# Optimization experiments

Hardware: AMD Instinct MI355X
Metric: run time of the kernel (lower is better)

## Reference

```python
import jax, jax.numpy as jnp
import numpy as np

CM = 0.05   # collision_margin
NT = 4      # n_timesteps

def _lin(x, W, b):
    return x @ W + b

def _mlp2(x, W1, b1, W2, b2):
    return _lin(jax.nn.relu(_lin(x, W1, b1)), W2, b2)

def _mlp3(x, W1, b1, W2, b2, W3, b3):
    h = jax.nn.relu(_lin(x, W1, b1))
    h = jax.nn.relu(_lin(h, W2, b2))
    return _lin(h, W3, b3)

def _xavier(key, fan_in, fan_out):
    std = np.sqrt(2.0 / (fan_in + fan_out))
    return jax.random.normal(key, (fan_in, fan_out), dtype=jnp.float32) * std

def setup_inputs() -> dict:
    key = jax.random.key(0)
    ks = jax.random.split(key, 16)
    sd, h, es, ud, rd, gd = 8, 128, 128, 32, 64, 32
    B, N, T = 16, 64, 8
    inp = {
        'states': jax.random.normal(ks[0], (B, N, T, sd), dtype=jnp.float32),
        'temp': 1,
        # StateEncoder: Linear(sd,h)-ReLU-Linear(h,es)-ReLU
        'sW1': _xavier(ks[1], sd, h), 'sb1': jnp.zeros((h,), jnp.float32),
        'sW2': _xavier(ks[2], h, es), 'sb2': jnp.zeros((es,), jnp.float32),
        # InputEncoder (collision_margin path): Linear(sd,h)-ReLU-Linear(h,ud)
        'uW1': _xavier(ks[3], sd, h), 'ub1': jnp.zeros((h,), jnp.float32),
        'uW2': _xavier(ks[4], h, ud), 'ub2': jnp.zeros((ud,), jnp.float32),
        # InputPropagator: Linear(es+ud, ud)
        'upW': _xavier(ks[5], es + ud, ud), 'upb': jnp.zeros((ud,), jnp.float32),
        # RelationEncoder (collision_margin path): Linear(sd,h)-ReLU-Linear(h,rd)
        'reW1': _xavier(ks[6], sd, h), 'reb1': jnp.zeros((h,), jnp.float32),
        'reW2': _xavier(ks[7], h, rd), 'reb2': jnp.zeros((rd,), jnp.float32),
        # RelationPropagator: Linear(2*es+rd, rd)
        'rpW': _xavier(ks[8], 2 * es + rd, rd), 'rpb': jnp.zeros((rd,), jnp.float32),
        # ComposedEmbedding: Linear(es+ud+rd,h)-ReLU-Linear(h,h)-ReLU-Linear(h,gd)
        'cW1': _xavier(ks[9], es + ud + rd, h), 'cb1': jnp.zeros((h,), jnp.float32),
        'cW2': _xavier(ks[10], h, h), 'cb2': jnp.zeros((h,), jnp.float32),
        'cW3': _xavier(ks[11], h, gd), 'cb3': jnp.zeros((gd,), jnp.float32),
    }
    return inp

def reference(states, temp, sW1, sb1, sW2, sb2, uW1, ub1, uW2, ub2, upW, upb,
              reW1, reb1, reW2, reb2, rpW, rpb, cW1, cb1, cW2, cb2, cW3, cb3):
    B, N, T, sd = states.shape
    BT = B * T
    s = states.transpose(0, 2, 1, 3).reshape(BT, N, sd)  # [BT,N,sd]

    # node encoders
    enc_obj = jax.nn.relu(_mlp2(s, sW1, sb1, sW2, sb2))   # [BT,N,es]
    enc_u = _mlp2(s, uW1, ub1, uW2, ub2)                  # [BT,N,ud] (no relu in collision_margin path)
    # u mask (get_u_states_mask)
    u = ((jnp.abs(s[..., 0:1]) > 1 - CM) | (jnp.abs(s[..., NT:NT + 1]) > 1 - CM)).astype(s.dtype)

    obs_u = jax.nn.relu(_lin(jnp.concatenate([enc_obj, enc_u], axis=-1), upW, upb))  # [BT,N,ud]
    enc_comp = jnp.concatenate([enc_obj, obs_u], axis=-1)  # [BT,N,es+ud]

    # pairwise relations: receiver i (dim1), sender j (dim2)
    rel_states = s[:, :, None, :] - s[:, None, :, :]        # [BT,N,N,sd]
    enc_rel = jax.nn.relu(_mlp2(rel_states, reW1, reb1, reW2, reb2))  # [BT,N,N,rd]
    sel = ((jnp.abs(rel_states[..., 0:1]) > 2 * CM) |
           (jnp.abs(rel_states[..., NT:NT + 1]) > 2 * CM)).astype(s.dtype)  # [BT,N,N,1]

    es = enc_obj.shape[-1]
    recv = jnp.broadcast_to(enc_obj[:, :, None, :], (BT, N, N, es))
    send = jnp.broadcast_to(enc_obj[:, None, :, :], (BT, N, N, es))
    rel_in = jnp.concatenate([recv, send, enc_rel], axis=-1)            # [BT,N,N,2es+rd]
    rel_eff = jax.nn.relu(_lin(rel_in, rpW, rpb)) * sel                 # [BT,N,N,rd]
    rel_agg = rel_eff.sum(axis=2)                                       # scatter-sum over senders -> [BT,N,rd]

    enc_comp = jnp.concatenate([enc_comp, rel_agg], axis=-1)            # [BT,N,es+ud+rd]
    g = _mlp3(enc_comp, cW1, cb1, cW2, cb2, cW3, cb3)                   # [BT,N,gd]
    return g.reshape(B, T, N, -1)
```

## Files before the change

### kernel.cpp

```cpp
#include <hip/hip_runtime.h>
#include <hip/hip_bf16.h>


typedef __bf16 bf16x8 __attribute__((ext_vector_type(8)));
typedef float f32x4 __attribute__((ext_vector_type(4)));

__global__ __launch_bounds__(256) void k_prep(
    const float* __restrict__ sW1, const float* __restrict__ uW1,
    const float* __restrict__ reW1, const float* __restrict__ sW2,
    const float* __restrict__ uW2, const float* __restrict__ upW,
    const float* __restrict__ reW2, const float* __restrict__ rpW,
    const float* __restrict__ cW1, const float* __restrict__ cW2,
    const float* __restrict__ cW3,
    __bf16* __restrict__ Wl1f, __bf16* __restrict__ Ws2f,
    __bf16* __restrict__ Wu2f, __bf16* __restrict__ Wupf,
    __bf16* __restrict__ Wabf, __bf16* __restrict__ W2f,
    __bf16* __restrict__ Wbf,  __bf16* __restrict__ Wc1f,
    __bf16* __restrict__ Wc2f, __bf16* __restrict__ Wc3f)
{
    const int tid  = blockIdx.x * 256 + threadIdx.x;
    const int nthr = gridDim.x * 256;

#define PACK(dst, NKT, NCT, EXPR)                                   \
    for (int q = tid; q < (NKT) * (NCT) * 512; q += nthr) {         \
        const int f = q >> 9, rem = q & 511;                        \
        const int lane = rem >> 3, e = rem & 7;                     \
        const int kt = f / (NCT), ct = f % (NCT);                   \
        const int k = kt * 32 + (lane >> 4) * 8 + e;                \
        const int c = ct * 16 + (lane & 15);                        \
        (dst)[q] = (__bf16)(EXPR);                                  \
        (void)k; (void)c;                                           \
    }

    PACK(Wl1f, 1, 24, (k >= 8 ? 0.f :
        (c < 128 ? sW1[k * 128 + c] :
         c < 256 ? uW1[k * 128 + (c - 128)] : reW1[k * 128 + (c - 256)])))
    PACK(Ws2f, 4, 8, sW2[k * 128 + c])
    PACK(Wu2f, 4, 2, uW2[k * 32 + c])
    PACK(Wupf, 5, 2, (k < 160 ? upW[k * 32 + c] : 0.f))
    PACK(Wabf, 4, 8, (c < 64 ? rpW[k * 64 + c] : rpW[(128 + k) * 64 + (c - 64)]))
    PACK(W2f,  4, 4, reW2[k * 64 + c])
    PACK(Wbf,  2, 4, rpW[(256 + k) * 64 + c])
    PACK(Wc1f, 7, 8, cW1[k * 128 + c])
    PACK(Wc2f, 4, 8, cW2[k * 128 + c])
    PACK(Wc3f, 4, 2, cW3[k * 32 + c])
#undef PACK
}

__global__ __launch_bounds__(256) void k_node(
    const float* __restrict__ states,
    const float* __restrict__ sb1, const float* __restrict__ sb2,
    const float* __restrict__ ub1, const float* __restrict__ ub2,
    const float* __restrict__ upb,
    const __bf16* __restrict__ Wl1f, const __bf16* __restrict__ Ws2f,
    const __bf16* __restrict__ Wu2f, const __bf16* __restrict__ Wupf,
    const __bf16* __restrict__ Wabf,
    float* __restrict__ P_g, float* __restrict__ A_g,
    __bf16* __restrict__ Bmh_g, __bf16* __restrict__ x_g)
{
    const int t = threadIdx.x;
    const int lane = t & 63;
    const int w = t >> 6;
    const int lr = lane >> 4, lc = lane & 15;
    const int nb = blockIdx.x * 16;

    __shared__ __bf16 s_h1hu[16 * 256];
    __shared__ __bf16 s_eoeu[16 * 192];

    bf16x8 af1 = {};
    if (lr == 0) {
        const int rg = nb + lc;
        const int bt = rg >> 6, n = rg & 63;
        const int b = bt >> 3, ts = bt & 7;
        const float* sp = &states[((size_t)((b * 64 + n) * 8 + ts)) * 8];
        const float4 s0 = *reinterpret_cast<const float4*>(sp);
        const float4 s1 = *reinterpret_cast<const float4*>(sp + 4);
        af1[0] = (__bf16)s0.x; af1[1] = (__bf16)s0.y;
        af1[2] = (__bf16)s0.z; af1[3] = (__bf16)s0.w;
        af1[4] = (__bf16)s1.x; af1[5] = (__bf16)s1.y;
        af1[6] = (__bf16)s1.z; af1[7] = (__bf16)s1.w;
    }

    #pragma unroll
    for (int ci = 0; ci < 6; ++ci) {
        const int ct = w * 6 + ci;
        const bf16x8 wf = *reinterpret_cast<const bf16x8*>(
            Wl1f + ((size_t)(ct * 64 + lane)) * 8);
        const float bias = (ct < 8) ? sb1[ct * 16 + lc]
                          : (ct < 16) ? ub1[(ct - 8) * 16 + lc] : 0.f;
        f32x4 acc = {bias, bias, bias, bias};
        acc = __builtin_amdgcn_mfma_f32_16x16x32_bf16(af1, wf, acc, 0, 0, 0);
        #pragma unroll
        for (int r = 0; r < 4; ++r) {
            const int jj = lr * 4 + r;
            if (ct < 16) {
                const int col = ct * 16 + lc;
                const int g = col >> 3;
                s_h1hu[jj * 256 + (((g ^ (jj & 7)) << 3) | (col & 7))] =
                    (__bf16)fmaxf(acc[r], 0.f);
            } else {
                P_g[(size_t)(nb + jj) * 128 + (ct - 16) * 16 + lc] = acc[r];
            }
        }
    }
    __syncthreads();

    const int jr = lc;
    const int sw = lc & 7;
    bf16x8 h1f[4];
    #pragma unroll
    for (int kt = 0; kt < 4; ++kt)
        h1f[kt] = *reinterpret_cast<const bf16x8*>(
            &s_h1hu[jr * 256 + (((kt * 4 + lr) ^ sw) << 3)]);
    #pragma unroll
    for (int ci = 0; ci < 2; ++ci) {
        const int ct = w * 2 + ci;
        const float bias = sb2[ct * 16 + lc];
        f32x4 acc = {bias, bias, bias, bias};
        #pragma unroll
        for (int kt = 0; kt < 4; ++kt) {
            const bf16x8 wf = *reinterpret_cast<const bf16x8*>(
                Ws2f + ((size_t)((kt * 8 + ct) * 64 + lane)) * 8);
            acc = __builtin_amdgcn_mfma_f32_16x16x32_bf16(h1f[kt], wf, acc, 0, 0, 0);
        }
        #pragma unroll
        for (int r = 0; r < 4; ++r) {
            const int jj = lr * 4 + r;
            const int col = ct * 16 + lc;
            const __bf16 v = (__bf16)fmaxf(acc[r], 0.f);
            x_g[(size_t)(nb + jj) * 160 + col] = v;
            const int g = col >> 3;
            s_eoeu[jj * 192 + (((g ^ (jj & 7)) << 3) | (col & 7))] = v;
        }
    }
    if (w < 2) {
        bf16x8 huf[4];
        #pragma unroll
        for (int kt = 0; kt < 4; ++kt)
            huf[kt] = *reinterpret_cast<const bf16x8*>(
                &s_h1hu[jr * 256 + (((16 + kt * 4 + lr) ^ sw) << 3)]);
        const int ct = w;
        const float bias = ub2[ct * 16 + lc];
        f32x4 acc = {bias, bias, bias, bias};
        #pragma unroll
        for (int kt = 0; kt < 4; ++kt) {
            const bf16x8 wf = *reinterpret_cast<const bf16x8*>(
                Wu2f + ((size_t)((kt * 2 + ct) * 64 + lane)) * 8);
            acc = __builtin_amdgcn_mfma_f32_16x16x32_bf16(huf[kt], wf, acc, 0, 0, 0);
        }
        #pragma unroll
        for (int r = 0; r < 4; ++r) {
            const int jj = lr * 4 + r;
            const int col = 128 + ct * 16 + lc;
            const int g = col >> 3;
            s_eoeu[jj * 192 + (((g ^ (jj & 7)) << 3) | (col & 7))] = (__bf16)acc[r];
        }
    }
    __syncthreads();

    bf16x8 eof[5];
    #pragma unroll
    for (int kt = 0; kt < 4; ++kt)
        eof[kt] = *reinterpret_cast<const bf16x8*>(
            &s_eoeu[jr * 192 + (((kt * 4 + lr) ^ sw) << 3)]);
    eof[4] = *reinterpret_cast<const bf16x8*>(
        &s_eoeu[jr * 192 + (((16 + lr) ^ sw) << 3)]);

    if (w < 2) {
        const int ct = w;
        const float bias = upb[ct * 16 + lc];
        f32x4 acc = {bias, bias, bias, bias};
        #pragma unroll
        for (int kt = 0; kt < 5; ++kt) {
            const bf16x8 wf = *reinterpret_cast<const bf16x8*>(
                Wupf + ((size_t)((kt * 2 + ct) * 64 + lane)) * 8);
            acc = __builtin_amdgcn_mfma_f32_16x16x32_bf16(eof[kt], wf, acc, 0, 0, 0);
        }
        #pragma unroll
        for (int r = 0; r < 4; ++r) {
            const int rg = nb + lr * 4 + r;
            x_g[(size_t)rg * 160 + 128 + ct * 16 + lc] = (__bf16)fmaxf(acc[r], 0.f);
        }
    }
    const int ab0 = (w < 2) ? w : 2 + (w - 2) * 3;
    const int abn = (w < 2) ? 1 : 3;
    for (int ci = 0; ci < abn; ++ci) {
        const int ct = ab0 + ci;
        f32x4 acc = {0.f, 0.f, 0.f, 0.f};
        #pragma unroll
        for (int kt = 0; kt < 4; ++kt) {
            const bf16x8 wf = *reinterpret_cast<const bf16x8*>(
                Wabf + ((size_t)((kt * 8 + ct) * 64 + lane)) * 8);
            acc = __builtin_amdgcn_mfma_f32_16x16x32_bf16(eof[kt], wf, acc, 0, 0, 0);
        }
        #pragma unroll
        for (int r = 0; r < 4; ++r) {
            const int rg = nb + lr * 4 + r;
            if (ct < 4) A_g[(size_t)rg * 64 + ct * 16 + lc] = acc[r];
            else        Bmh_g[(size_t)rg * 64 + (ct - 4) * 16 + lc] = (__bf16)acc[r];
        }
    }
}

__global__ __launch_bounds__(256, 2) void k_pair(
    const float* __restrict__ states,
    const float* __restrict__ P_g, const float* __restrict__ A_g,
    const __bf16* __restrict__ Bmh_g,
    const float* __restrict__ reb1, const float* __restrict__ reb2,
    const float* __restrict__ rpb,
    const __bf16* __restrict__ W2f, const __bf16* __restrict__ Wbf,
    float* __restrict__ relagg_g)
{
    const int t    = threadIdx.x;
    const int lane = t & 63;
    const int w    = t >> 6;
    const int lr   = lane >> 4;
    const int lc   = lane & 15;
    const int bid  = (blockIdx.x & 7) * 64 + (blockIdx.x >> 3);
    const int bt   = bid >> 2;
    const int ig   = bid & 3;
    const int b    = bt >> 3, tstep = bt & 7;

    __shared__ float  s_pj[64 * 128];
    __shared__ __bf16 s_er[4][16 * 64];
    __shared__ __bf16 s_bm[64 * 72];
    __shared__ float  s_ai[16 * 64];
    __shared__ float  s_rb[128];
    __shared__ float  s_s0[64], s_s4[64];

    for (int idx = t; idx < 2048; idx += 256) {
        const int j = idx >> 5, f = idx & 31;
        const float4 v = *reinterpret_cast<const float4*>(
            &P_g[(size_t)(bt * 64 + j) * 128 + f * 4]);
        *reinterpret_cast<float4*>(&s_pj[j * 128 + ((f ^ (j & 7)) << 2)]) = v;
    }
    for (int idx = t; idx < 512; idx += 256) {
        const int j = idx >> 3, c8 = (idx & 7) * 8;
        *reinterpret_cast<bf16x8*>(&s_bm[j * 72 + c8]) =
            *reinterpret_cast<const bf16x8*>(&Bmh_g[(size_t)(bt * 64 + j) * 64 + c8]);
    }
    for (int idx = t; idx < 1024; idx += 256) {
        const int il = idx >> 6, c = idx & 63;
        s_ai[idx] = A_g[(size_t)(bt * 64 + ig * 16 + il) * 64 + c] + rpb[c];
    }
    if (t < 128) s_rb[t] = reb1[t];
    if (t < 64) {
        const float* sp = &states[((size_t)((b * 64 + t) * 8 + tstep)) * 8];
        s_s0[t] = sp[0];
        s_s4[t] = sp[4];
    }

    bf16x8 w2f[4][4];
    #pragma unroll
    for (int kt = 0; kt < 4; ++kt)
        #pragma unroll
        for (int ct = 0; ct < 4; ++ct)
            w2f[kt][ct] = *reinterpret_cast<const bf16x8*>(
                W2f + ((size_t)((kt * 4 + ct) * 64 + lane)) * 8);
    bf16x8 wbf[2][4];
    #pragma unroll
    for (int kt = 0; kt < 2; ++kt)
        #pragma unroll
        for (int ct = 0; ct < 4; ++ct)
            wbf[kt][ct] = *reinterpret_cast<const bf16x8*>(
                Wbf + ((size_t)((kt * 4 + ct) * 64 + lane)) * 8);
    float reb2c[4];
    #pragma unroll
    for (int ct = 0; ct < 4; ++ct) reb2c[ct] = reb2[ct * 16 + lc];

    __syncthreads();

    __bf16* er = s_er[w];

    for (int q = 0; q < 4; ++q) {
        const int il = w * 4 + q;
        const int i  = ig * 16 + il;
        const int isw = i & 7;

        float4 pib[4][2];
        #pragma unroll
        for (int kt = 0; kt < 4; ++kt) {
            const int f0 = kt * 8 + lr * 2;
            const float4 p0 = *reinterpret_cast<const float4*>(
                &s_pj[i * 128 + ((f0 ^ isw) << 2)]);
            const float4 p1 = *reinterpret_cast<const float4*>(
                &s_pj[i * 128 + (((f0 + 1) ^ isw) << 2)]);
            const int kb = kt * 32 + lr * 8;
            const float4 r0 = *reinterpret_cast<const float4*>(&s_rb[kb]);
            const float4 r1 = *reinterpret_cast<const float4*>(&s_rb[kb + 4]);
            pib[kt][0].x = p0.x + r0.x; pib[kt][0].y = p0.y + r0.y;
            pib[kt][0].z = p0.z + r0.z; pib[kt][0].w = p0.w + r0.w;
            pib[kt][1].x = p1.x + r1.x; pib[kt][1].y = p1.y + r1.y;
            pib[kt][1].z = p1.z + r1.z; pib[kt][1].w = p1.w + r1.w;
        }
        float aic[4];
        #pragma unroll
        for (int ct = 0; ct < 4; ++ct) aic[ct] = s_ai[il * 64 + ct * 16 + lc];
        const unsigned long long selm = __ballot(
            fabsf(s_s0[i] - s_s0[lane]) > 0.1f ||
            fabsf(s_s4[i] - s_s4[lane]) > 0.1f);

        float ragg[4] = {0.f, 0.f, 0.f, 0.f};

        for (int jt = 0; jt < 4; ++jt) {
            const int j = jt * 16 + lc;
            const int jsw = j & 7;
            bf16x8 af[4];
            #pragma unroll
            for (int kt = 0; kt < 4; ++kt) {
                const int f0 = kt * 8 + lr * 2;
                const float4 p0 = *reinterpret_cast<const float4*>(
                    &s_pj[j * 128 + ((f0 ^ jsw) << 2)]);
                const float4 p1 = *reinterpret_cast<const float4*>(
                    &s_pj[j * 128 + (((f0 + 1) ^ jsw) << 2)]);
                bf16x8 a;
                a[0] = (__bf16)fmaxf(pib[kt][0].x - p0.x, 0.f);
                a[1] = (__bf16)fmaxf(pib[kt][0].y - p0.y, 0.f);
                a[2] = (__bf16)fmaxf(pib[kt][0].z - p0.z, 0.f);
                a[3] = (__bf16)fmaxf(pib[kt][0].w - p0.w, 0.f);
                a[4] = (__bf16)fmaxf(pib[kt][1].x - p1.x, 0.f);
                a[5] = (__bf16)fmaxf(pib[kt][1].y - p1.y, 0.f);
                a[6] = (__bf16)fmaxf(pib[kt][1].z - p1.z, 0.f);
                a[7] = (__bf16)fmaxf(pib[kt][1].w - p1.w, 0.f);
                af[kt] = a;
            }
            #pragma unroll
            for (int ct = 0; ct < 4; ++ct) {
                f32x4 acc = {reb2c[ct], reb2c[ct], reb2c[ct], reb2c[ct]};
                #pragma unroll
                for (int kt = 0; kt < 4; ++kt)
                    acc = __builtin_amdgcn_mfma_f32_16x16x32_bf16(
                        af[kt], w2f[kt][ct], acc, 0, 0, 0);
                #pragma unroll
                for (int r = 0; r < 4; ++r) {
                    const int jj2 = lr * 4 + r;
                    const int c = ct * 16 + lc;
                    er[jj2 * 64 + ((((c >> 3) ^ (jj2 & 7)) << 3) | (c & 7))] =
                        (__bf16)fmaxf(acc[r], 0.f);
                }
            }
            bf16x8 a2[2];
            #pragma unroll
            for (int kt = 0; kt < 2; ++kt) {
                const int g = (kt * 4 + lr) ^ (lc & 7);
                a2[kt] = *reinterpret_cast<const bf16x8*>(&er[lc * 64 + (g << 3)]);
            }
            #pragma unroll
            for (int ct = 0; ct < 4; ++ct) {
                f32x4 acc = {aic[ct], aic[ct], aic[ct], aic[ct]};
                #pragma unroll
                for (int kt = 0; kt < 2; ++kt)
                    acc = __builtin_amdgcn_mfma_f32_16x16x32_bf16(
                        a2[kt], wbf[kt][ct], acc, 0, 0, 0);
                #pragma unroll
                for (int r = 0; r < 4; ++r) {
                    const int jj = jt * 16 + lr * 4 + r;
                    const float bm = (float)s_bm[jj * 72 + ct * 16 + lc];
                    float v = fmaxf(acc[r] + bm, 0.f);
                    v = ((selm >> jj) & 1ull) ? v : 0.f;
                    ragg[ct] += v;
                }
            }
        }
        #pragma unroll
        for (int ct = 0; ct < 4; ++ct) {
            ragg[ct] += __shfl_xor(ragg[ct], 16);
            ragg[ct] += __shfl_xor(ragg[ct], 32);
        }
        if (lr == 0) {
            #pragma unroll
            for (int ct = 0; ct < 4; ++ct)
                relagg_g[(size_t)(bt * 64 + i) * 64 + ct * 16 + lc] = ragg[ct];
        }
    }
}

__global__ __launch_bounds__(256) void k_comp(
    const __bf16* __restrict__ x_g, const float* __restrict__ relagg_g,
    const float* __restrict__ cb1, const float* __restrict__ cb2,
    const float* __restrict__ cb3,
    const __bf16* __restrict__ Wc1f, const __bf16* __restrict__ Wc2f,
    const __bf16* __restrict__ Wc3f,
    float* __restrict__ out)
{
    const int t = threadIdx.x;
    const int lane = t & 63;
    const int w = t >> 6;
    const int lr = lane >> 4, lc = lane & 15;
    const int nb = blockIdx.x * 16;

    __shared__ __bf16 s_x[16 * 256];
    __shared__ __bf16 s_h1[16 * 128];
    __shared__ __bf16 s_h2[16 * 128];

    for (int idx = t; idx < 320; idx += 256) {
        const int j = idx / 20, g = idx - j * 20;
        const bf16x8 v = *reinterpret_cast<const bf16x8*>(
            x_g + (size_t)(nb + j) * 160 + g * 8);
        *reinterpret_cast<bf16x8*>(&s_x[j * 256 + ((g ^ (j & 7)) << 3)]) = v;
    }
    {
        const int j = t >> 4, c4 = (t & 15) * 4;
        const float4 v = *reinterpret_cast<const float4*>(
            &relagg_g[(size_t)(nb + j) * 64 + c4]);
        union { __bf16 bb[4]; uint2 u; } pk;
        pk.bb[0] = (__bf16)v.x; pk.bb[1] = (__bf16)v.y;
        pk.bb[2] = (__bf16)v.z; pk.bb[3] = (__bf16)v.w;
        const int g = 20 + (c4 >> 3);
        *reinterpret_cast<uint2*>(
            &s_x[j * 256 + ((g ^ (j & 7)) << 3) + (c4 & 7)]) = pk.u;
    }
    __syncthreads();

    const int jr = lc;
    const int sw = lc & 7;
    bf16x8 xf[7];
    #pragma unroll
    for (int kt = 0; kt < 7; ++kt)
        xf[kt] = *reinterpret_cast<const bf16x8*>(
            &s_x[jr * 256 + (((kt * 4 + lr) ^ sw) << 3)]);
    #pragma unroll
    for (int ci = 0; ci < 2; ++ci) {
        const int ct = w * 2 + ci;
        const float bias = cb1[ct * 16 + lc];
        f32x4 acc = {bias, bias, bias, bias};
        #pragma unroll
        for (int kt = 0; kt < 7; ++kt) {
            const bf16x8 wf = *reinterpret_cast<const bf16x8*>(
                Wc1f + ((size_t)((kt * 8 + ct) * 64 + lane)) * 8);
            acc = __builtin_amdgcn_mfma_f32_16x16x32_bf16(xf[kt], wf, acc, 0, 0, 0);
        }
        #pragma unroll
        for (int r = 0; r < 4; ++r) {
            const int jj = lr * 4 + r;
            const int col = ct * 16 + lc, g = col >> 3;
            s_h1[jj * 128 + (((g ^ (jj & 7)) << 3) | (col & 7))] =
                (__bf16)fmaxf(acc[r], 0.f);
        }
    }
    __syncthreads();

    bf16x8 hf[4];
    #pragma unroll
    for (int kt = 0; kt < 4; ++kt)
        hf[kt] = *reinterpret_cast<const bf16x8*>(
            &s_h1[jr * 128 + (((kt * 4 + lr) ^ sw) << 3)]);
    #pragma unroll
    for (int ci = 0; ci < 2; ++ci) {
        const int ct = w * 2 + ci;
        const float bias = cb2[ct * 16 + lc];
        f32x4 acc = {bias, bias, bias, bias};
        #pragma unroll
        for (int kt = 0; kt < 4; ++kt) {
            const bf16x8 wf = *reinterpret_cast<const bf16x8*>(
                Wc2f + ((size_t)((kt * 8 + ct) * 64 + lane)) * 8);
            acc = __builtin_amdgcn_mfma_f32_16x16x32_bf16(hf[kt], wf, acc, 0, 0, 0);
        }
        #pragma unroll
        for (int r = 0; r < 4; ++r) {
            const int jj = lr * 4 + r;
            const int col = ct * 16 + lc, g = col >> 3;
            s_h2[jj * 128 + (((g ^ (jj & 7)) << 3) | (col & 7))] =
                (__bf16)fmaxf(acc[r], 0.f);
        }
    }
    __syncthreads();

    if (w < 2) {
        bf16x8 h2f[4];
        #pragma unroll
        for (int kt = 0; kt < 4; ++kt)
            h2f[kt] = *reinterpret_cast<const bf16x8*>(
                &s_h2[jr * 128 + (((kt * 4 + lr) ^ sw) << 3)]);
        const int ct = w;
        const float bias = cb3[ct * 16 + lc];
        f32x4 acc = {bias, bias, bias, bias};
        #pragma unroll
        for (int kt = 0; kt < 4; ++kt) {
            const bf16x8 wf = *reinterpret_cast<const bf16x8*>(
                Wc3f + ((size_t)((kt * 2 + ct) * 64 + lane)) * 8);
            acc = __builtin_amdgcn_mfma_f32_16x16x32_bf16(h2f[kt], wf, acc, 0, 0, 0);
        }
        #pragma unroll
        for (int r = 0; r < 4; ++r) {
            const int rg = nb + lr * 4 + r;
            out[(size_t)rg * 32 + ct * 16 + lc] = acc[r];
        }
    }
}

extern "C" void kernel_launch(void* const* d_in, const int* in_sizes, int n_in,
                              void* d_out, int out_size, void* d_ws, size_t ws_size,
                              hipStream_t stream) {
    const float* states = (const float*)d_in[0];
    const float* sW1  = (const float*)d_in[2];
    const float* sb1  = (const float*)d_in[3];
    const float* sW2  = (const float*)d_in[4];
    const float* sb2  = (const float*)d_in[5];
    const float* uW1  = (const float*)d_in[6];
    const float* ub1  = (const float*)d_in[7];
    const float* uW2  = (const float*)d_in[8];
    const float* ub2  = (const float*)d_in[9];
    const float* upW  = (const float*)d_in[10];
    const float* upb  = (const float*)d_in[11];
    const float* reW1 = (const float*)d_in[12];
    const float* reb1 = (const float*)d_in[13];
    const float* reW2 = (const float*)d_in[14];
    const float* reb2 = (const float*)d_in[15];
    const float* rpW  = (const float*)d_in[16];
    const float* rpb  = (const float*)d_in[17];
    const float* cW1  = (const float*)d_in[18];
    const float* cb1  = (const float*)d_in[19];
    const float* cW2  = (const float*)d_in[20];
    const float* cb2  = (const float*)d_in[21];
    const float* cW3  = (const float*)d_in[22];
    const float* cb3  = (const float*)d_in[23];
    float* out = (float*)d_out;

    float* ws = (float*)d_ws;
    float* P_g      = ws;
    float* A_g      = P_g + 8192 * 128;
    float* relagg_g = A_g + 8192 * 64;
    __bf16* x_g   = (__bf16*)(relagg_g + 8192 * 64);
    __bf16* Bmh_g = x_g + 8192 * 160;
    __bf16* Wl1f  = Bmh_g + 8192 * 64;
    __bf16* Ws2f  = Wl1f + 24 * 512;
    __bf16* Wu2f  = Ws2f + 32 * 512;
    __bf16* Wupf  = Wu2f + 8 * 512;
    __bf16* Wabf  = Wupf + 10 * 512;
    __bf16* W2f   = Wabf + 32 * 512;
    __bf16* Wbf   = W2f + 16 * 512;
    __bf16* Wc1f  = Wbf + 8 * 512;
    __bf16* Wc2f  = Wc1f + 56 * 512;
    __bf16* Wc3f  = Wc2f + 32 * 512;

    k_prep<<<64, 256, 0, stream>>>(sW1, uW1, reW1, sW2, uW2, upW, reW2, rpW,
                                   cW1, cW2, cW3,
                                   Wl1f, Ws2f, Wu2f, Wupf, Wabf, W2f, Wbf,
                                   Wc1f, Wc2f, Wc3f);
    k_node<<<512, 256, 0, stream>>>(states, sb1, sb2, ub1, ub2, upb,
                                    Wl1f, Ws2f, Wu2f, Wupf, Wabf,
                                    P_g, A_g, Bmh_g, x_g);
    k_pair<<<512, 256, 0, stream>>>(states, P_g, A_g, Bmh_g,
                                    reb1, reb2, rpb, W2f, Wbf, relagg_g);
    k_comp<<<512, 256, 0, stream>>>(x_g, relagg_g, cb1, cb2, cb3,
                                    Wc1f, Wc2f, Wc3f, out);
}
```

Baseline: 159.9 us.

## Fuse pair and composition kernels, switch pair path to fp16 packed math

Merges the pairwise relation kernel with the composed-embedding MLP so rel_agg stays in registers and shared memory instead of making a round trip through global memory. The pair path now uses fp16 storage and packed half8 subtract/ReLU with f16 MFMA, replacing the per-element fp32-to-bf16 conversion, and the P buffer moves from fp32 to fp16 to halve its traffic. Both node and fused kernels now run 512-thread blocks with less work per wave. Risks include fp16 range and precision limits, and occupancy pressure from the launch bound of 6 blocks at 512 threads.

Result: slower. 295.8 us (+85.1%).

```diff
diff --git a/kernel.cpp b/kernel.cpp
--- a/kernel.cpp
+++ b/kernel.cpp
@@ -3,7 +3,13 @@
 
 
 typedef __bf16 bf16x8 __attribute__((ext_vector_type(8)));
+typedef _Float16 half8 __attribute__((ext_vector_type(8)));
 typedef float f32x4 __attribute__((ext_vector_type(4)));
+
+static __device__ __forceinline__ half8 relu8(half8 x) {
+    half8 z = {};
+    return __builtin_elementwise_max(x, z);
+}
 
 __global__ __launch_bounds__(256) void k_prep(
     const float* __restrict__ sW1, const float* __restrict__ uW1,
@@ -14,40 +20,40 @@
     const float* __restrict__ cW3,
     __bf16* __restrict__ Wl1f, __bf16* __restrict__ Ws2f,
     __bf16* __restrict__ Wu2f, __bf16* __restrict__ Wupf,
-    __bf16* __restrict__ Wabf, __bf16* __restrict__ W2f,
-    __bf16* __restrict__ Wbf,  __bf16* __restrict__ Wc1f,
+    __bf16* __restrict__ Wabf, _Float16* __restrict__ W2f,
+    _Float16* __restrict__ Wbf, __bf16* __restrict__ Wc1f,
     __bf16* __restrict__ Wc2f, __bf16* __restrict__ Wc3f)
 {
     const int tid  = blockIdx.x * 256 + threadIdx.x;
     const int nthr = gridDim.x * 256;
 
-#define PACK(dst, NKT, NCT, EXPR)                                   \
+#define PACK(dst, CAST, NKT, NCT, EXPR)                             \
     for (int q = tid; q < (NKT) * (NCT) * 512; q += nthr) {         \
         const int f = q >> 9, rem = q & 511;                        \
         const int lane = rem >> 3, e = rem & 7;                     \
         const int kt = f / (NCT), ct = f % (NCT);                   \
         const int k = kt * 32 + (lane >> 4) * 8 + e;                \
         const int c = ct * 16 + (lane & 15);                        \
-        (dst)[q] = (__bf16)(EXPR);                                  \
+        (dst)[q] = (CAST)(EXPR);                                    \
         (void)k; (void)c;                                           \
     }
 
-    PACK(Wl1f, 1, 24, (k >= 8 ? 0.f :
+    PACK(Wl1f, __bf16, 1, 24, (k >= 8 ? 0.f :
         (c < 128 ? sW1[k * 128 + c] :
          c < 256 ? uW1[k * 128 + (c - 128)] : reW1[k * 128 + (c - 256)])))
-    PACK(Ws2f, 4, 8, sW2[k * 128 + c])
-    PACK(Wu2f, 4, 2, uW2[k * 32 + c])
-    PACK(Wupf, 5, 2, (k < 160 ? upW[k * 32 + c] : 0.f))
-    PACK(Wabf, 4, 8, (c < 64 ? rpW[k * 64 + c] : rpW[(128 + k) * 64 + (c - 64)]))
-    PACK(W2f,  4, 4, reW2[k * 64 + c])
-    PACK(Wbf,  2, 4, rpW[(256 + k) * 64 + c])
-    PACK(Wc1f, 7, 8, cW1[k * 128 + c])
-    PACK(Wc2f, 4, 8, cW2[k * 128 + c])
-    PACK(Wc3f, 4, 2, cW3[k * 32 + c])
+    PACK(Ws2f, __bf16, 4, 8, sW2[k * 128 + c])
+    PACK(Wu2f, __bf16, 4, 2, uW2[k * 32 + c])
+    PACK(Wupf, __bf16, 5, 2, (k < 160 ? upW[k * 32 + c] : 0.f))
+    PACK(Wabf, __bf16, 4, 8, (c < 64 ? rpW[k * 64 + c] : rpW[(128 + k) * 64 + (c - 64)]))
+    PACK(W2f,  _Float16, 4, 4, reW2[k * 64 + c])
+    PACK(Wbf,  _Float16, 2, 4, rpW[(256 + k) * 64 + c])
+    PACK(Wc1f, __bf16, 7, 8, cW1[k * 128 + c])
+    PACK(Wc2f, __bf16, 4, 8, cW2[k * 128 + c])
+    PACK(Wc3f, __bf16, 4, 2, cW3[k * 32 + c])
 #undef PACK
 }
 
-__global__ __launch_bounds__(256) void k_node(
+__global__ __launch_bounds__(512) void k_node(
     const float* __restrict__ states,
     const float* __restrict__ sb1, const float* __restrict__ sb2,
     const float* __restrict__ ub1, const float* __restrict__ ub2,
@@ -55,8 +61,8 @@
     const __bf16* __restrict__ Wl1f, const __bf16* __restrict__ Ws2f,
     const __bf16* __restrict__ Wu2f, const __bf16* __restrict__ Wupf,
     const __bf16* __restrict__ Wabf,
-    float* __restrict__ P_g, float* __restrict__ A_g,
-    __bf16* __restrict__ Bmh_g, __bf16* __restrict__ x_g)
+    _Float16* __restrict__ P_h, float* __restrict__ A_g,
+    _Float16* __restrict__ Bh_g, __bf16* __restrict__ x_g)
 {
     const int t = threadIdx.x;
     const int lane = t & 63;
@@ -82,8 +88,8 @@
     }
 
     #pragma unroll
-    for (int ci = 0; ci < 6; ++ci) {
-        const int ct = w * 6 + ci;
+    for (int ci = 0; ci < 3; ++ci) {
+        const int ct = w * 3 + ci;
         const bf16x8 wf = *reinterpret_cast<const bf16x8*>(
             Wl1f + ((size_t)(ct * 64 + lane)) * 8);
         const float bias = (ct < 8) ? sb1[ct * 16 + lc]
@@ -99,7 +105,8 @@
                 s_h1hu[jj * 256 + (((g ^ (jj & 7)) << 3) | (col & 7))] =
                     (__bf16)fmaxf(acc[r], 0.f);
             } else {
-                P_g[(size_t)(nb + jj) * 128 + (ct - 16) * 16 + lc] = acc[r];
+                P_h[(size_t)(nb + jj) * 128 + (ct - 16) * 16 + lc] =
+                    (_Float16)acc[r];
             }
         }
     }
@@ -112,9 +119,8 @@
     for (int kt = 0; kt < 4; ++kt)
         h1f[kt] = *reinterpret_cast<const bf16x8*>(
             &s_h1hu[jr * 256 + (((kt * 4 + lr) ^ sw) << 3)]);
-    #pragma unroll
-    for (int ci = 0; ci < 2; ++ci) {
-        const int ct = w * 2 + ci;
+    {
+        const int ct = w;
         const float bias = sb2[ct * 16 + lc];
         f32x4 acc = {bias, bias, bias, bias};
         #pragma unroll
@@ -166,8 +172,8 @@
     eof[4] = *reinterpret_cast<const bf16x8*>(
         &s_eoeu[jr * 192 + (((16 + lr) ^ sw) << 3)]);
 
-    if (w < 2) {
-        const int ct = w;
+    if (w >= 6) {
+        const int ct = w - 6;
         const float bias = upb[ct * 16 + lc];
         f32x4 acc = {bias, bias, bias, bias};
         #pragma unroll
@@ -182,10 +188,8 @@
             x_g[(size_t)rg * 160 + 128 + ct * 16 + lc] = (__bf16)fmaxf(acc[r], 0.f);
         }
     }
-    const int ab0 = (w < 2) ? w : 2 + (w - 2) * 3;
-    const int abn = (w < 2) ? 1 : 3;
-    for (int ci = 0; ci < abn; ++ci) {
-        const int ct = ab0 + ci;
+    {
+        const int ct = w;
         f32x4 acc = {0.f, 0.f, 0.f, 0.f};
         #pragma unroll
         for (int kt = 0; kt < 4; ++kt) {
@@ -197,19 +201,23 @@
         for (int r = 0; r < 4; ++r) {
             const int rg = nb + lr * 4 + r;
             if (ct < 4) A_g[(size_t)rg * 64 + ct * 16 + lc] = acc[r];
-            else        Bmh_g[(size_t)rg * 64 + (ct - 4) * 16 + lc] = (__bf16)acc[r];
+            else        Bh_g[(size_t)rg * 64 + (ct - 4) * 16 + lc] = (_Float16)acc[r];
         }
     }
 }
 
-__global__ __launch_bounds__(256, 2) void k_pair(
+__global__ __launch_bounds__(512, 6) void k_pairc(
     const float* __restrict__ states,
-    const float* __restrict__ P_g, const float* __restrict__ A_g,
-    const __bf16* __restrict__ Bmh_g,
+    const _Float16* __restrict__ P_h, const float* __restrict__ A_g,
+    const _Float16* __restrict__ Bh_g, const __bf16* __restrict__ x_g,
     const float* __restrict__ reb1, const float* __restrict__ reb2,
     const float* __restrict__ rpb,
-    const __bf16* __restrict__ W2f, const __bf16* __restrict__ Wbf,
-    float* __restrict__ relagg_g)
+    const _Float16* __restrict__ W2f, const _Float16* __restrict__ Wbf,
+    const float* __restrict__ cb1, const float* __restrict__ cb2,
+    const float* __restrict__ cb3,
+    const __bf16* __restrict__ Wc1f, const __bf16* __restrict__ Wc2f,
+    const __bf16* __restrict__ Wc3f,
+    float* __restrict__ out)
 {
     const int t    = threadIdx.x;
     const int lane = t & 63;
@@ -220,49 +228,52 @@
     const int bt   = bid >> 2;
     const int ig   = bid & 3;
     const int b    = bt >> 3, tstep = bt & 7;
-
-    __shared__ float  s_pj[64 * 128];
-    __shared__ __bf16 s_er[4][16 * 64];
-    __shared__ __bf16 s_bm[64 * 72];
-    __shared__ float  s_ai[16 * 64];
-    __shared__ float  s_rb[128];
-    __shared__ float  s_s0[64], s_s4[64];
-
-    for (int idx = t; idx < 2048; idx += 256) {
-        const int j = idx >> 5, f = idx & 31;
-        const float4 v = *reinterpret_cast<const float4*>(
-            &P_g[(size_t)(bt * 64 + j) * 128 + f * 4]);
-        *reinterpret_cast<float4*>(&s_pj[j * 128 + ((f ^ (j & 7)) << 2)]) = v;
-    }
-    for (int idx = t; idx < 512; idx += 256) {
-        const int j = idx >> 3, c8 = (idx & 7) * 8;
-        *reinterpret_cast<bf16x8*>(&s_bm[j * 72 + c8]) =
-            *reinterpret_cast<const bf16x8*>(&Bmh_g[(size_t)(bt * 64 + j) * 64 + c8]);
-    }
-    for (int idx = t; idx < 1024; idx += 256) {
+    const int rowb = bt * 64 + ig * 16;
+
+    __shared__ _Float16 s_pj[64 * 128];
+    __shared__ _Float16 s_er[8][16 * 64];
+    __shared__ _Float16 s_bm[64 * 72];
+    __shared__ float    s_ai[16 * 64];
+    __shared__ _Float16 s_rb[128];
+    __shared__ float    s_s0[64], s_s4[64];
+
+    for (int idx = t; idx < 1024; idx += 512) {
+        const int j = idx >> 4, g = idx & 15;
+        const half8 v = *reinterpret_cast<const half8*>(
+            P_h + (size_t)(bt * 64 + j) * 128 + g * 8);
+        *reinterpret_cast<half8*>(&s_pj[j * 128 + ((g ^ (j & 7)) << 3)]) = v;
+    }
+    {
+        const int j = t >> 3, c8 = (t & 7) * 8;
+        if (t < 512)
+            *reinterpret_cast<half8*>(&s_bm[j * 72 + c8]) =
+                *reinterpret_cast<const half8*>(
+                    Bh_g + (size_t)(bt * 64 + j) * 64 + c8);
+    }
+    for (int idx = t; idx < 1024; idx += 512) {
         const int il = idx >> 6, c = idx & 63;
-        s_ai[idx] = A_g[(size_t)(bt * 64 + ig * 16 + il) * 64 + c] + rpb[c];
-    }
-    if (t < 128) s_rb[t] = reb1[t];
+        s_ai[idx] = A_g[(size_t)(rowb + il) * 64 + c] + rpb[c];
+    }
+    if (t < 128) s_rb[t] = (_Float16)reb1[t];
     if (t < 64) {
         const float* sp = &states[((size_t)((b * 64 + t) * 8 + tstep)) * 8];
         s_s0[t] = sp[0];
         s_s4[t] = sp[4];
     }
 
-    bf16x8 w2f[4][4];
+    half8 w2f[4][4];
     #pragma unroll
     for (int kt = 0; kt < 4; ++kt)
         #pragma unroll
         for (int ct = 0; ct < 4; ++ct)
-            w2f[kt][ct] = *reinterpret_cast<const bf16x8*>(
+            w2f[kt][ct] = *reinterpret_cast<const half8*>(
                 W2f + ((size_t)((kt * 4 + ct) * 64 + lane)) * 8);
-    bf16x8 wbf[2][4];
+    half8 wbf[2][4];
     #pragma unroll
     for (int kt = 0; kt < 2; ++kt)
         #pragma unroll
         for (int ct = 0; ct < 4; ++ct)
-            wbf[kt][ct] = *reinterpret_cast<const bf16x8*>(
+            wbf[kt][ct] = *reinterpret_cast<const half8*>(
                 Wbf + ((size_t)((kt * 4 + ct) * 64 + lane)) * 8);
     float reb2c[4];
     #pragma unroll
@@ -270,28 +281,22 @@
 
     __syncthreads();
 
-    __bf16* er = s_er[w];
-
-    for (int q = 0; q < 4; ++q) {
-        const int il = w * 4 + q;
+    _Float16* er = s_er[w];
+    float rag2[2][4];
+
+    for (int q = 0; q < 2; ++q) {
+        const int il = w * 2 + q;
         const int i  = ig * 16 + il;
         const int isw = i & 7;
 
-        float4 pib[4][2];
+        half8 pib[4];
         #pragma unroll
         for (int kt = 0; kt < 4; ++kt) {
-            const int f0 = kt * 8 + lr * 2;
-            const float4 p0 = *reinterpret_cast<const float4*>(
-                &s_pj[i * 128 + ((f0 ^ isw) << 2)]);
-            const float4 p1 = *reinterpret_cast<const float4*>(
-                &s_pj[i * 128 + (((f0 + 1) ^ isw) << 2)]);
-            const int kb = kt * 32 + lr * 8;
-            const float4 r0 = *reinterpret_cast<const float4*>(&s_rb[kb]);
-            const float4 r1 = *reinterpret_cast<const float4*>(&s_rb[kb + 4]);
-            pib[kt][0].x = p0.x + r0.x; pib[kt][0].y = p0.y + r0.y;
-            pib[kt][0].z = p0.z + r0.z; pib[kt][0].w = p0.w + r0.w;
-            pib[kt][1].x = p1.x + r1.x; pib[kt][1].y = p1.y + r1.y;
-            pib[kt][1].z = p1.z + r1.z; pib[kt][1].w = p1.w + r1.w;
+            const int g = kt * 4 + lr;
+            const half8 pv = *reinterpret_cast<const half8*>(
+                &s_pj[i * 128 + ((g ^ isw) << 3)]);
+            const half8 rb = *reinterpret_cast<const half8*>(&s_rb[g * 8]);
+            pib[kt] = pv + rb;
         }
         float aic[4];
         #pragma unroll
@@ -305,52 +310,41 @@
         for (int jt = 0; jt < 4; ++jt) {
             const int j = jt * 16 + lc;
             const int jsw = j & 7;
-            bf16x8 af[4];
+            half8 af[4];
             #pragma unroll
             for (int kt = 0; kt < 4; ++kt) {
-                const int f0 = kt * 8 + lr * 2;
-                const float4 p0 = *reinterpret_cast<const float4*>(
-                    &s_pj[j * 128 + ((f0 ^ jsw) << 2)]);
-                const float4 p1 = *reinterpret_cast<const float4*>(
-                    &s_pj[j * 128 + (((f0 + 1) ^ jsw) << 2)]);
-                bf16x8 a;
-                a[0] = (__bf16)fmaxf(pib[kt][0].x - p0.x, 0.f);
-                a[1] = (__bf16)fmaxf(pib[kt][0].y - p0.y, 0.f);
-                a[2] = (__bf16)fmaxf(pib[kt][0].z - p0.z, 0.f);
-                a[3] = (__bf16)fmaxf(pib[kt][0].w - p0.w, 0.f);
-                a[4] = (__bf16)fmaxf(pib[kt][1].x - p1.x, 0.f);
-                a[5] = (__bf16)fmaxf(pib[kt][1].y - p1.y, 0.f);
-                a[6] = (__bf16)fmaxf(pib[kt][1].z - p1.z, 0.f);
-                a[7] = (__bf16)fmaxf(pib[kt][1].w - p1.w, 0.f);
-                af[kt] = a;
+                const int g = (kt * 4 + lr) ^ jsw;
+                const half8 pj = *reinterpret_cast<const half8*>(
+                    &s_pj[j * 128 + (g << 3)]);
+                af[kt] = relu8(pib[kt] - pj);
             }
             #pragma unroll
             for (int ct = 0; ct < 4; ++ct) {
                 f32x4 acc = {reb2c[ct], reb2c[ct], reb2c[ct], reb2c[ct]};
                 #pragma unroll
                 for (int kt = 0; kt < 4; ++kt)
-                    acc = __builtin_amdgcn_mfma_f32_16x16x32_bf16(
+                    acc = __builtin_amdgcn_mfma_f32_16x16x32_f16(
                         af[kt], w2f[kt][ct], acc, 0, 0, 0);
                 #pragma unroll
                 for (int r = 0; r < 4; ++r) {
                     const int jj2 = lr * 4 + r;
                     const int c = ct * 16 + lc;
                     er[jj2 * 64 + ((((c >> 3) ^ (jj2 & 7)) << 3) | (c & 7))] =
-                        (__bf16)fmaxf(acc[r], 0.f);
+                        (_Float16)fmaxf(acc[r], 0.f);
                 }
             }
-            bf16x8 a2[2];
+            half8 a2[2];
             #pragma unroll
             for (int kt = 0; kt < 2; ++kt) {
                 const int g = (kt * 4 + lr) ^ (lc & 7);
-                a2[kt] = *reinterpret_cast<const bf16x8*>(&er[lc * 64 + (g << 3)]);
+                a2[kt] = *reinterpret_cast<const half8*>(&er[lc * 64 + (g << 3)]);
             }
             #pragma unroll
             for (int ct = 0; ct < 4; ++ct) {
                 f32x4 acc = {aic[ct], aic[ct], aic[ct], aic[ct]};
                 #pragma unroll
                 for (int kt = 0; kt < 2; ++kt)
-                    acc = __builtin_amdgcn_mfma_f32_16x16x32_bf16(
+                    acc = __builtin_amdgcn_mfma_f32_16x16x32_f16(
                         a2[kt], wbf[kt][ct], acc, 0, 0, 0);
                 #pragma unroll
                 for (int r = 0; r < 4; ++r) {
@@ -366,49 +360,33 @@
         for (int ct = 0; ct < 4; ++ct) {
             ragg[ct] += __shfl_xor(ragg[ct], 16);
             ragg[ct] += __shfl_xor(ragg[ct], 32);
-        }
-        if (lr == 0) {
-            #pragma unroll
-            for (int ct = 0; ct < 4; ++ct)
-                relagg_g[(size_t)(bt * 64 + i) * 64 + ct * 16 + lc] = ragg[ct];
-        }
-    }
-}
-
-__global__ __launch_bounds__(256) void k_comp(
-    const __bf16* __restrict__ x_g, const float* __restrict__ relagg_g,
-    const float* __restrict__ cb1, const float* __restrict__ cb2,
-    const float* __restrict__ cb3,
-    const __bf16* __restrict__ Wc1f, const __bf16* __restrict__ Wc2f,
-    const __bf16* __restrict__ Wc3f,
-    float* __restrict__ out)
-{
-    const int t = threadIdx.x;
-    const int lane = t & 63;
-    const int w = t >> 6;
-    const int lr = lane >> 4, lc = lane & 15;
-    const int nb = blockIdx.x * 16;
-
-    __shared__ __bf16 s_x[16 * 256];
-    __shared__ __bf16 s_h1[16 * 128];
-    __shared__ __bf16 s_h2[16 * 128];
-
-    for (int idx = t; idx < 320; idx += 256) {
+            rag2[q][ct] = ragg[ct];
+        }
+    }
+    __syncthreads();
+
+    __bf16* s_x  = reinterpret_cast<__bf16*>(s_pj);
+    __bf16* s_h1 = s_x + 16 * 256;
+    __bf16* s_h2 = s_h1 + 16 * 128;
+
+    for (int idx = t; idx < 320; idx += 512) {
         const int j = idx / 20, g = idx - j * 20;
         const bf16x8 v = *reinterpret_cast<const bf16x8*>(
-            x_g + (size_t)(nb + j) * 160 + g * 8);
+            x_g + (size_t)(rowb + j) * 160 + g * 8);
         *reinterpret_cast<bf16x8*>(&s_x[j * 256 + ((g ^ (j & 7)) << 3)]) = v;
     }
-    {
-        const int j = t >> 4, c4 = (t & 15) * 4;
-        const float4 v = *reinterpret_cast<const float4*>(
-            &relagg_g[(size_t)(nb + j) * 64 + c4]);
-        union { __bf16 bb[4]; uint2 u; } pk;
-        pk.bb[0] = (__bf16)v.x; pk.bb[1] = (__bf16)v.y;
-        pk.bb[2] = (__bf16)v.z; pk.bb[3] = (__bf16)v.w;
-        const int g = 20 + (c4 >> 3);
-        *reinterpret_cast<uint2*>(
-            &s_x[j * 256 + ((g ^ (j & 7)) << 3) + (c4 & 7)]) = pk.u;
+    if (lr == 0) {
+        #pragma unroll
+        for (int q = 0; q < 2; ++q) {
+            const int il = w * 2 + q;
+            #pragma unroll
+            for (int ct = 0; ct < 4; ++ct) {
+                const int c = ct * 16 + lc;
+                const int gg = 20 + (c >> 3);
+                s_x[il * 256 + ((gg ^ (il & 7)) << 3) + (c & 7)] =
+                    (__bf16)rag2[q][ct];
+            }
+        }
     }
     __syncthreads();
 
@@ -419,9 +397,8 @@
     for (int kt = 0; kt < 7; ++kt)
         xf[kt] = *reinterpret_cast<const bf16x8*>(
             &s_x[jr * 256 + (((kt * 4 + lr) ^ sw) << 3)]);
-    #pragma unroll
-    for (int ci = 0; ci < 2; ++ci) {
-        const int ct = w * 2 + ci;
+    {
+        const int ct = w;
         const float bias = cb1[ct * 16 + lc];
         f32x4 acc = {bias, bias, bias, bias};
         #pragma unroll
@@ -445,9 +422,8 @@
     for (int kt = 0; kt < 4; ++kt)
         hf[kt] = *reinterpret_cast<const bf16x8*>(
             &s_h1[jr * 128 + (((kt * 4 + lr) ^ sw) << 3)]);
-    #pragma unroll
-    for (int ci = 0; ci < 2; ++ci) {
-        const int ct = w * 2 + ci;
+    {
+        const int ct = w;
         const float bias = cb2[ct * 16 + lc];
         f32x4 acc = {bias, bias, bias, bias};
         #pragma unroll
@@ -483,7 +459,7 @@
         }
         #pragma unroll
         for (int r = 0; r < 4; ++r) {
-            const int rg = nb + lr * 4 + r;
+            const int rg = rowb + lr * 4 + r;
             out[(size_t)rg * 32 + ct * 16 + lc] = acc[r];
         }
     }
@@ -518,31 +494,29 @@
     float* out = (float*)d_out;
 
     float* ws = (float*)d_ws;
-    float* P_g      = ws;
-    float* A_g      = P_g + 8192 * 128;
-    float* relagg_g = A_g + 8192 * 64;
-    __bf16* x_g   = (__bf16*)(relagg_g + 8192 * 64);
-    __bf16* Bmh_g = x_g + 8192 * 160;
-    __bf16* Wl1f  = Bmh_g + 8192 * 64;
-    __bf16* Ws2f  = Wl1f + 24 * 512;
-    __bf16* Wu2f  = Ws2f + 32 * 512;
-    __bf16* Wupf  = Wu2f + 8 * 512;
-    __bf16* Wabf  = Wupf + 10 * 512;
-    __bf16* W2f   = Wabf + 32 * 512;
-    __bf16* Wbf   = W2f + 16 * 512;
-    __bf16* Wc1f  = Wbf + 8 * 512;
-    __bf16* Wc2f  = Wc1f + 56 * 512;
-    __bf16* Wc3f  = Wc2f + 32 * 512;
+    float* A_g = ws;
+    _Float16* P_h  = (_Float16*)(A_g + 8192 * 64);
+    _Float16* Bh_g = P_h + 8192 * 128;
+    _Float16* W2f  = Bh_g + 8192 * 64;
+    _Float16* Wbf  = W2f + 16 * 512;
+    __bf16* x_g  = (__bf16*)(Wbf + 8 * 512);
+    __bf16* Wl1f = x_g + 8192 * 160;
+    __bf16* Ws2f = Wl1f + 24 * 512;
+    __bf16* Wu2f = Ws2f + 32 * 512;
+    __bf16* Wupf = Wu2f + 8 * 512;
+    __bf16* Wabf = Wupf + 10 * 512;
+    __bf16* Wc1f = Wabf + 32 * 512;
+    __bf16* Wc2f = Wc1f + 56 * 512;
+    __bf16* Wc3f = Wc2f + 32 * 512;
 
     k_prep<<<64, 256, 0, stream>>>(sW1, uW1, reW1, sW2, uW2, upW, reW2, rpW,
                                    cW1, cW2, cW3,
                                    Wl1f, Ws2f, Wu2f, Wupf, Wabf, W2f, Wbf,
                                    Wc1f, Wc2f, Wc3f);
-    k_node<<<512, 256, 0, stream>>>(states, sb1, sb2, ub1, ub2, upb,
+    k_node<<<512, 512, 0, stream>>>(states, sb1, sb2, ub1, ub2, upb,
                                     Wl1f, Ws2f, Wu2f, Wupf, Wabf,
-                                    P_g, A_g, Bmh_g, x_g);
-    k_pair<<<512, 256, 0, stream>>>(states, P_g, A_g, Bmh_g,
-                                    reb1, reb2, rpb, W2f, Wbf, relagg_g);
-    k_comp<<<512, 256, 0, stream>>>(x_g, relagg_g, cb1, cb2, cb3,
-                                    Wc1f, Wc2f, Wc3f, out);
+                                    P_h, A_g, Bh_g, x_g);
+    k_pairc<<<512, 512, 0, stream>>>(states, P_h, A_g, Bh_g, x_g,
+                                     reb1, reb2, rpb, W2f, Wbf,
+                                     cb1, cb2, cb3, Wc1f, Wc2f, Wc3f, out);
 }
```
